# Performance work log

Measured on AMD Instinct MI355X. Metric: run time of the kernel, lower is better.

Reference implementation:

```python
import math
import jax, jax.numpy as jnp
import numpy as np

B, S, D, H = 2, 2048, 1024, 16


def setup_inputs() -> dict:
    key = jax.random.key(0)
    ks = jax.random.split(key, 8)
    scale = 1.0 / math.sqrt(D)
    kv_mask = jax.random.randint(ks[1], (B, S), 0, 2).astype(bool)
    kv_mask = kv_mask.at[:, 0].set(True)  # ensure at least one valid kv per batch
    return {
        "q": jax.random.normal(ks[0], (B, S, D), dtype=jnp.float32),
        "kv_mask": kv_mask,
        "Wq": jax.random.normal(ks[2], (D, D), dtype=jnp.float32) * scale,
        "Wk": jax.random.normal(ks[3], (D, D), dtype=jnp.float32) * scale,
        "Wv": jax.random.normal(ks[4], (D, D), dtype=jnp.float32) * scale,
        "Wo": jax.random.normal(ks[5], (D, D), dtype=jnp.float32) * scale,
        "bo": jax.random.normal(ks[6], (D,), dtype=jnp.float32) * 0.01,
        "num_heads": H,
    }


def _pass_with_mask(x, W, mask, b=None):
    # Linear applied everywhere, output zeroed where mask is False (pass_with_mask)
    y = x @ W.T
    if b is not None:
        y = y + b
    return jnp.where(mask[..., None], y, 0.0)


def reference(q, kv_mask, Wq, Wk, Wv, Wo, bo, num_heads):
    b, s, d = q.shape
    hd = d // num_heads
    q_mask = jnp.ones((b, s), dtype=bool)  # default q_mask in the module
    # self-attention: k = v = q
    qh = _pass_with_mask(q, Wq, q_mask).reshape(b, s, num_heads, hd)
    kh = _pass_with_mask(q, Wk, kv_mask).reshape(b, s, num_heads, hd)
    vh = _pass_with_mask(q, Wv, kv_mask).reshape(b, s, num_heads, hd)
    # scores: note the module scales by sqrt(model_dim), NOT sqrt(head_dim)
    scores = jnp.einsum("bqhd,bkhd->bhqk", qh, kh) / math.sqrt(d)
    mask = (q_mask[:, :, None] & kv_mask[:, None, :])[:, None, :, :]  # [b,1,q,k]
    scores = jnp.where(mask, scores, -jnp.inf)
    attn = jax.nn.softmax(scores, axis=-1)
    attn = jnp.where(mask, attn, 0.0)
    out = jnp.einsum("bhqk,bkhd->bqhd", attn, vh).reshape(b, s, d)
    return _pass_with_mask(out, Wo, q_mask, bo)
```

## Files before the change

### kernel.cpp

```cpp
#include <hip/hip_runtime.h>
#include <math.h>

#define B_ 2
#define S_ 2048
#define DM 1024
#define NH 16
#define HD 64

typedef unsigned short u16;
typedef unsigned int u32;
typedef __attribute__((ext_vector_type(8))) short bf16x8;
typedef __attribute__((ext_vector_type(4))) float f32x4;

#define C2SCALE 0.0450842200277800f

__device__ __forceinline__ u16 f2bf(float x) {
  unsigned u = __float_as_uint(x);
  u = (u + 0x7FFFu + ((u >> 16) & 1u)) >> 16;
  return (u16)u;
}

__device__ __forceinline__ u32 cvtpk(float lo, float hi) {
  u32 r;
  asm("v_cvt_pk_bf16_f32 %0, %1, %2" : "=v"(r) : "v"(lo), "v"(hi));
  return r;
}

__device__ __forceinline__ float exp2a(float x) {
  float r;
  asm("v_exp_f32 %0, %1" : "=v"(r) : "v"(x));
  return r;
}

__device__ __forceinline__ void gload_lds16(const u16* g, u16* l) {
  __builtin_amdgcn_global_load_lds((const __attribute__((address_space(1))) void*)g,
                                   (__attribute__((address_space(3))) void*)l, 16, 0, 0);
}

__device__ __forceinline__ int sigpos(int w6) {
  return ((w6 >> 5) << 5) | (((w6 >> 2) & 3) << 3) | (((w6 >> 4) & 1) << 2) | (w6 & 3);
}

__global__ void mask_scan(const int* __restrict__ kvm, int* __restrict__ posb,
                          int* __restrict__ nvb, u16* __restrict__ mwg) {
  const int b = blockIdx.x;
  const int tid = threadIdx.x;
  const int lane = tid & 63, wv = tid >> 6;
  __shared__ int wsum[4];
  int v[8], s = 0;
  const int base = b * S_ + tid * 8;
#pragma unroll
  for (int j = 0; j < 8; j++) { v[j] = kvm[base + j] ? 1 : 0; s += v[j]; }
  int sc = s;
#pragma unroll
  for (int off = 1; off < 64; off <<= 1) {
    int t = __shfl_up(sc, off, 64);
    if (lane >= off) sc += t;
  }
  if (lane == 63) wsum[wv] = sc;
  __syncthreads();
  int woff = 0;
#pragma unroll
  for (int w = 0; w < 4; w++) woff += (w < wv) ? wsum[w] : 0;
  int run = woff + sc - s;
#pragma unroll
  for (int j = 0; j < 8; j++) { posb[base + j] = run; run += v[j]; }
  const int total = wsum[0] + wsum[1] + wsum[2] + wsum[3];
  if (tid == 0) nvb[b] = total;
  for (int i = tid; i < S_; i += 256)
    mwg[b * S_ + (i & ~63) + sigpos(i & 63)] = (i < total) ? 0xFFFFu : 0u;
}

__global__ void cvt_all(const float* __restrict__ q, const float* __restrict__ Wq,
                        const float* __restrict__ Wk, const float* __restrict__ Wv,
                        const float* __restrict__ Wo, const int* __restrict__ kvm,
                        const int* __restrict__ posb, const int* __restrict__ nvb,
                        u16* __restrict__ Xbf, u16* __restrict__ Wcat,
                        u16* __restrict__ Wobf, u16* __restrict__ vtbuf,
                        u16* __restrict__ Xc) {
  const int NQ4 = (B_ * S_ * DM) / 4;
  const int NW4 = (DM * DM) / 4;
  const int total = NQ4 + 4 * NW4;
  int i = blockIdx.x * blockDim.x + threadIdx.x;
  int stride = gridDim.x * blockDim.x;
  for (int idx = i; idx < B_ * NH * HD * 64; idx += stride) {
    int col = idx & 63;
    int dd = (idx >> 6) & 63;
    int bh = idx >> 12;
    int nv = nvb[bh >> 4];
    int padw = ((nv + 63) & ~63) - nv;
    if (col < padw)
      vtbuf[((size_t)bh * HD + dd) * S_ + nv + col] = 0;
  }
  for (; i < total; i += stride) {
    if (i < NQ4) {
      float4 v = ((const float4*)q)[i];
      ushort4 o;
      o.x = f2bf(v.x); o.y = f2bf(v.y); o.z = f2bf(v.z); o.w = f2bf(v.w);
      ((ushort4*)Xbf)[i] = o;
      int row = i >> 8, chunk = i & 255;
      int b = row >> 11, s = row & 2047;
      if (kvm[b * S_ + s]) {
        int p = posb[b * S_ + s];
        *(ushort4*)(Xc + ((size_t)(b * S_ + p)) * DM + chunk * 4) = o;
      }
    } else {
      int t = i - NQ4;
      const float* src;
      u16* dst;
      if (t < NW4)            { src = Wq + (size_t)t * 4; dst = Wcat + (size_t)t * 4; }
      else if (t < 2 * NW4)   { src = Wk + (size_t)(t - NW4) * 4;     dst = Wcat + DM * DM + (size_t)(t - NW4) * 4; }
      else if (t < 3 * NW4)   { src = Wv + (size_t)(t - 2 * NW4) * 4; dst = Wcat + 2 * DM * DM + (size_t)(t - 2 * NW4) * 4; }
      else                    { src = Wo + (size_t)(t - 3 * NW4) * 4; dst = Wobf + (size_t)(t - 3 * NW4) * 4; }
      float4 v = *(const float4*)src;
      ushort4 o;
      o.x = f2bf(v.x); o.y = f2bf(v.y); o.z = f2bf(v.z); o.w = f2bf(v.w);
      *(ushort4*)dst = o;
    }
  }
}

__global__ __launch_bounds__(512, 4) void gemm_qkv(
    const u16* __restrict__ Xbf, const u16* __restrict__ Xc,
    const u16* __restrict__ Wcat, u16* __restrict__ qo, u16* __restrict__ ko,
    u16* __restrict__ vo, const int* __restrict__ nvb) {
  const int K = DM;
  const int Lraw = blockIdx.x;
  const int Ls = (Lraw & 7) * 96 + (Lraw >> 3);

  int Mb, nglob, bkv = 0, nv = 1 << 30;
  const u16* Ap;
  if (Ls < 256) {
    Mb = (Ls & 31) << 7;
    nglob = (Ls >> 5) << 7;
    Ap = Xbf;
  } else {
    int L2 = Ls - 256;
    bkv = L2 >> 8;
    int L3 = L2 & 255;
    Mb = (L3 & 15) << 7;
    nglob = 1024 + ((L3 >> 4) << 7);
    nv = nvb[bkv];
    if (Mb >= nv) return;
    Ap = Xc + (size_t)bkv * S_ * DM;
  }

  __shared__ __align__(16) u16 As[2][128 * 64];
  __shared__ __align__(16) u16 Bs[2][128 * 64];
  const int tid = threadIdx.x;
  const int wv = tid >> 6, lane = tid & 63;
  const int g = lane >> 4, c = lane & 15;
  const int wr = wv >> 1, wc = wv & 1;

  f32x4 acc[2][4];
#pragma unroll
  for (int i = 0; i < 2; i++)
#pragma unroll
    for (int j = 0; j < 4; j++) acc[i][j] = f32x4{0.f, 0.f, 0.f, 0.f};

  const int r1 = tid >> 3;
  const int col8 = tid & 7;
  const u16* ag1 = Ap + (size_t)(Mb + r1) * K + col8 * 8;
  const u16* ag2 = ag1 + (size_t)64 * K;
  const u16* bg1 = Wcat + (size_t)(nglob + r1) * K + col8 * 8;
  const u16* bg2 = bg1 + (size_t)64 * K;
  const int slot = col8 ^ (r1 & 7);
  u16* al1 = &As[0][r1 * 64 + slot * 8];
  u16* al2 = al1 + 64 * 64;
  u16* bl1 = &Bs[0][r1 * 64 + slot * 8];
  u16* bl2 = bl1 + 64 * 64;

  bf16x8 ar0 = *(const bf16x8*)ag1, ar1 = *(const bf16x8*)ag2;
  bf16x8 br0 = *(const bf16x8*)bg1, br1 = *(const bf16x8*)bg2;
  *(bf16x8*)al1 = ar0; *(bf16x8*)al2 = ar1;
  *(bf16x8*)bl1 = br0; *(bf16x8*)bl2 = br1;
  ar0 = *(const bf16x8*)(ag1 + 64); ar1 = *(const bf16x8*)(ag2 + 64);
  br0 = *(const bf16x8*)(bg1 + 64); br1 = *(const bf16x8*)(bg2 + 64);
  __syncthreads();

  const int swz = c & 7;
  const int NTI = 16;

  for (int t = 0; t < NTI; ++t) {
    const int cur = t & 1;
    if (t + 1 < NTI) {
      const int nb = (cur ^ 1) * 8192;
      *(bf16x8*)(al1 + nb) = ar0; *(bf16x8*)(al2 + nb) = ar1;
      *(bf16x8*)(bl1 + nb) = br0; *(bf16x8*)(bl2 + nb) = br1;
      if (t + 2 < NTI) {
        ar0 = *(const bf16x8*)(ag1 + (t + 2) * 64);
        ar1 = *(const bf16x8*)(ag2 + (t + 2) * 64);
        br0 = *(const bf16x8*)(bg1 + (t + 2) * 64);
        br1 = *(const bf16x8*)(bg2 + (t + 2) * 64);
      }
    }
    const u16* AB = &As[cur][0];
    const u16* BB = &Bs[cur][0];
#pragma unroll
    for (int ks = 0; ks < 2; ks++) {
      const int koff = ((4 * ks + g) ^ swz) * 8;
      bf16x8 af[2], bfr[4];
#pragma unroll
      for (int mi = 0; mi < 2; mi++)
        af[mi] = *(const bf16x8*)&AB[(wr * 32 + mi * 16 + c) * 64 + koff];
#pragma unroll
      for (int ni = 0; ni < 4; ni++)
        bfr[ni] = *(const bf16x8*)&BB[(wc * 64 + ni * 16 + c) * 64 + koff];
#pragma unroll
      for (int mi = 0; mi < 2; mi++)
#pragma unroll
        for (int ni = 0; ni < 4; ni++)
          acc[mi][ni] = __builtin_amdgcn_mfma_f32_16x16x32_bf16(af[mi], bfr[ni], acc[mi][ni], 0, 0, 0);
    }
    asm volatile("s_waitcnt lgkmcnt(0)\n\ts_barrier" ::: "memory");
  }

  const int nbase = nglob + wc * 64 + c;
  const int which = nbase >> 10;
  if (which == 0) {
#pragma unroll
    for (int mi = 0; mi < 2; mi++) {
#pragma unroll
      for (int ni = 0; ni < 4; ni++) {
        int nn = nbase + ni * 16;
        int h = nn >> 6, d = nn & 63;
#pragma unroll
        for (int r = 0; r < 4; r++) {
          int row = Mb + wr * 32 + mi * 16 + g * 4 + r;
          int b0 = row >> 11, s0 = row & 2047;
          qo[(((size_t)(b0 * NH + h)) * S_ + s0) * HD + d] =
              f2bf(acc[mi][ni][r] * C2SCALE);
        }
      }
    }
  } else if (which == 1) {
#pragma unroll
    for (int mi = 0; mi < 2; mi++) {
#pragma unroll
      for (int r = 0; r < 4; r++) {
        int p = Mb + wr * 32 + mi * 16 + g * 4 + r;
        if (p < nv) {
#pragma unroll
          for (int ni = 0; ni < 4; ni++) {
            int nn = (nbase + ni * 16) & 1023;
            ko[((size_t)(bkv * NH + (nn >> 6)) * S_ + p) * HD + (nn & 63)] =
                f2bf(acc[mi][ni][r]);
          }
        }
      }
    }
  } else {
#pragma unroll
    for (int mi = 0; mi < 2; mi++) {
#pragma unroll
      for (int r = 0; r < 4; r++) {
        int p = Mb + wr * 32 + mi * 16 + g * 4 + r;
        if (p < nv) {
          int dst = (p & ~63) + sigpos(p & 63);
#pragma unroll
          for (int ni = 0; ni < 4; ni++) {
            int nn = (nbase + ni * 16) & 1023;
            vo[((size_t)((bkv * NH + (nn >> 6)) * HD + (nn & 63))) * S_ + dst] =
                f2bf(acc[mi][ni][r]);
          }
        }
      }
    }
  }
}

__global__ __launch_bounds__(256, 4) void gemm_n64(
    const u16* __restrict__ A, const u16* __restrict__ Bw,
    const float* __restrict__ bias, float* __restrict__ fo) {
  __shared__ __align__(16) u16 As[128 * 32];
  __shared__ __align__(16) u16 Bs[64 * 32];
  const int K = DM, N = DM;
  const int tid = threadIdx.x;
  const int wv = tid >> 6, lane = tid & 63;
  const int g = lane >> 4, c = lane & 15;
  const int wr = wv >> 1, wc = wv & 1;
  const int L = blockIdx.x;
  const int Ls = (L & 7) * 64 + (L >> 3);
  const int Mb = (Ls & 31) << 7, Nb = (Ls >> 5) << 6;

  f32x4 acc[4][2];
#pragma unroll
  for (int i = 0; i < 4; i++)
#pragma unroll
    for (int j = 0; j < 2; j++) acc[i][j] = f32x4{0.f, 0.f, 0.f, 0.f};

  for (int kb = 0; kb < K; kb += 32) {
#pragma unroll
    for (int it = 0; it < 2; ++it) {
      int id = it * 256 + tid;
      int m = id >> 2, kk = (id & 3) * 8;
      gload_lds16(A + (size_t)(Mb + m) * K + kb + kk, As + (it * 4 + wv) * 512);
    }
    {
      int m = tid >> 2, kk = (tid & 3) * 8;
      gload_lds16(Bw + (size_t)(Nb + m) * K + kb + kk, Bs + wv * 512);
    }
    __syncthreads();
    bf16x8 af[4], bfr[2];
#pragma unroll
    for (int mi = 0; mi < 4; mi++)
      af[mi] = *(const bf16x8*)(As + (wr * 64 + mi * 16 + c) * 32 + g * 8);
#pragma unroll
    for (int ni = 0; ni < 2; ni++)
      bfr[ni] = *(const bf16x8*)(Bs + (wc * 32 + ni * 16 + c) * 32 + g * 8);
#pragma unroll
    for (int mi = 0; mi < 4; mi++)
#pragma unroll
      for (int ni = 0; ni < 2; ni++)
        acc[mi][ni] = __builtin_amdgcn_mfma_f32_16x16x32_bf16(af[mi], bfr[ni], acc[mi][ni], 0, 0, 0);
    __syncthreads();
  }

#pragma unroll
  for (int mi = 0; mi < 4; mi++) {
#pragma unroll
    for (int ni = 0; ni < 2; ni++) {
      int n = Nb + wc * 32 + ni * 16 + c;
      float bv = bias[n];
#pragma unroll
      for (int r = 0; r < 4; r++) {
        int row = Mb + wr * 64 + mi * 16 + g * 4 + r;
        fo[(size_t)row * N + n] = acc[mi][ni][r] + bv;
      }
    }
  }
}

__global__ __launch_bounds__(256, 3) void attn_kernel(
    const u16* __restrict__ qb, const u16* __restrict__ kb,
    const u16* __restrict__ vtb, const u16* __restrict__ mwg,
    const int* __restrict__ nvb, u16* __restrict__ ob) {
  __shared__ __align__(16) u16 Kl[2][64 * 64];
  __shared__ __align__(16) u16 Vl[2][64 * 64];
  __shared__ __align__(16) u16 MW[S_];

  const int tid = threadIdx.x;
  const int wv = tid >> 6, lane = tid & 63;
  const int g = lane >> 4, c = lane & 15;

  const int L = blockIdx.x;
  const int j = L >> 3;
  const int bh = ((L & 7) << 2) | (j >> 4);
  const int qi = j & 15;
  const int b = bh >> 4, h = bh & 15;
  const int q0 = qi * 128;
  const size_t bhbase = (size_t)bh * (S_ * HD);
  const int NT = (nvb[b] + 63) >> 6;

  ((uint4*)MW)[tid] = ((const uint4*)(mwg + b * S_))[tid];

  bf16x8 qf[2][2];
#pragma unroll
  for (int mi = 0; mi < 2; mi++)
#pragma unroll
    for (int ks = 0; ks < 2; ks++)
      qf[mi][ks] = *(const bf16x8*)(qb + bhbase +
                   (size_t)(q0 + wv * 32 + mi * 16 + c) * HD + ks * 32 + g * 8);

  f32x4 Oa[4][2];
#pragma unroll
  for (int di = 0; di < 4; di++)
#pragma unroll
    for (int mi = 0; mi < 2; mi++) Oa[di][mi] = f32x4{0.f, 0.f, 0.f, 0.f};
  f32x4 lacc[2];
  lacc[0] = f32x4{0.f, 0.f, 0.f, 0.f};
  lacc[1] = f32x4{0.f, 0.f, 0.f, 0.f};

  union { u32 u[4]; bf16x8 v; } ones;
#pragma unroll
  for (int w = 0; w < 4; w++) ones.u[w] = 0x3F803F80u;

  const int srow = tid >> 3;
  const int scol8 = tid & 7;
  const u16* kg1 = kb + bhbase + (size_t)srow * HD + scol8 * 8;
  const u16* kg2 = kg1 + (size_t)32 * HD;
  const u16* vg1 = vtb + bhbase + (size_t)srow * S_ + scol8 * 8;
  const u16* vg2 = vg1 + (size_t)32 * S_;
  const int wslot = scol8 ^ (srow & 7);
  u16* kld1 = &Kl[0][srow * 64 + wslot * 8];
  u16* kld2 = kld1 + 32 * 64;
  u16* vld1 = &Vl[0][srow * 64 + wslot * 8];
  u16* vld2 = vld1 + 32 * 64;

  bf16x8 krg[2], vrg[2];
  krg[0] = *(const bf16x8*)kg1;  krg[1] = *(const bf16x8*)kg2;
  vrg[0] = *(const bf16x8*)vg1;  vrg[1] = *(const bf16x8*)vg2;
  *(bf16x8*)kld1 = krg[0];  *(bf16x8*)kld2 = krg[1];
  *(bf16x8*)vld1 = vrg[0];  *(bf16x8*)vld2 = vrg[1];
  krg[0] = *(const bf16x8*)(kg1 + 4096);  krg[1] = *(const bf16x8*)(kg2 + 4096);
  vrg[0] = *(const bf16x8*)(vg1 + 64);    vrg[1] = *(const bf16x8*)(vg2 + 64);
  __syncthreads();

  const int swz = c & 7;

  for (int t = 0; t < NT; ++t) {
    const int cur = t & 1;
    if (t + 1 < NT) {
      const int nb = (cur ^ 1) * 4096;
      *(bf16x8*)(kld1 + nb) = krg[0];  *(bf16x8*)(kld2 + nb) = krg[1];
      *(bf16x8*)(vld1 + nb) = vrg[0];  *(bf16x8*)(vld2 + nb) = vrg[1];
      if (t + 2 < NT) {
        krg[0] = *(const bf16x8*)(kg1 + (t + 2) * 4096);
        krg[1] = *(const bf16x8*)(kg2 + (t + 2) * 4096);
        vrg[0] = *(const bf16x8*)(vg1 + (t + 2) * 64);
        vrg[1] = *(const bf16x8*)(vg2 + (t + 2) * 64);
      }
    }
    const u16* KB = &Kl[cur][0];
    const u16* VB = &Vl[cur][0];

    f32x4 Sa[4][2];
#pragma unroll
    for (int ni = 0; ni < 4; ni++)
#pragma unroll
      for (int mi = 0; mi < 2; mi++) Sa[ni][mi] = f32x4{0.f, 0.f, 0.f, 0.f};
    __builtin_amdgcn_s_setprio(1);
#pragma unroll
    for (int ks = 0; ks < 2; ks++) {
      bf16x8 kf[4];
#pragma unroll
      for (int ni = 0; ni < 4; ni++)
        kf[ni] = *(const bf16x8*)&KB[(ni * 16 + c) * 64 + (((4 * ks + g) ^ swz) * 8)];
#pragma unroll
      for (int ni = 0; ni < 4; ni++)
#pragma unroll
        for (int mi = 0; mi < 2; mi++)
          Sa[ni][mi] = __builtin_amdgcn_mfma_f32_16x16x32_bf16(kf[ni], qf[mi][ks], Sa[ni][mi], 0, 0, 0);
    }
    __builtin_amdgcn_s_setprio(0);

    bf16x8 Pa[2][2];
#pragma unroll
    for (int ks = 0; ks < 2; ks++) {
      uint4 mw = *(const uint4*)&MW[t * 64 + ks * 32 + g * 8];
#pragma unroll
      for (int mi = 0; mi < 2; mi++) {
        union { u32 u[4]; bf16x8 v; } pw;
        pw.u[0] = cvtpk(exp2a(Sa[2 * ks][mi][0]), exp2a(Sa[2 * ks][mi][1])) & mw.x;
        pw.u[1] = cvtpk(exp2a(Sa[2 * ks][mi][2]), exp2a(Sa[2 * ks][mi][3])) & mw.y;
        pw.u[2] = cvtpk(exp2a(Sa[2 * ks + 1][mi][0]), exp2a(Sa[2 * ks + 1][mi][1])) & mw.z;
        pw.u[3] = cvtpk(exp2a(Sa[2 * ks + 1][mi][2]), exp2a(Sa[2 * ks + 1][mi][3])) & mw.w;
        Pa[mi][ks] = pw.v;
      }
    }

    __builtin_amdgcn_s_setprio(1);
#pragma unroll
    for (int mi = 0; mi < 2; mi++) {
      lacc[mi] = __builtin_amdgcn_mfma_f32_16x16x32_bf16(ones.v, Pa[mi][0], lacc[mi], 0, 0, 0);
      lacc[mi] = __builtin_amdgcn_mfma_f32_16x16x32_bf16(ones.v, Pa[mi][1], lacc[mi], 0, 0, 0);
    }
#pragma unroll
    for (int ks = 0; ks < 2; ks++) {
      bf16x8 vf[4];
#pragma unroll
      for (int di = 0; di < 4; di++)
        vf[di] = *(const bf16x8*)&VB[(di * 16 + c) * 64 + (((4 * ks + g) ^ swz) * 8)];
#pragma unroll
      for (int di = 0; di < 4; di++)
#pragma unroll
        for (int mi = 0; mi < 2; mi++)
          Oa[di][mi] = __builtin_amdgcn_mfma_f32_16x16x32_bf16(vf[di], Pa[mi][ks], Oa[di][mi], 0, 0, 0);
    }
    __builtin_amdgcn_s_setprio(0);

    asm volatile("s_waitcnt lgkmcnt(0)\n\ts_barrier" ::: "memory");
  }

#pragma unroll
  for (int mi = 0; mi < 2; mi++) {
    float inv = 1.f / lacc[mi][0];
    int q = q0 + wv * 32 + mi * 16 + c;
    size_t base = ((size_t)(b * S_ + q)) * DM + (size_t)h * HD;
#pragma unroll
    for (int di = 0; di < 4; di++) {
      uint2 o;
      o.x = cvtpk(Oa[di][mi][0] * inv, Oa[di][mi][1] * inv);
      o.y = cvtpk(Oa[di][mi][2] * inv, Oa[di][mi][3] * inv);
      *(uint2*)(ob + base + di * 16 + g * 4) = o;
    }
  }
}

extern "C" void kernel_launch(void* const* d_in, const int* in_sizes, int n_in,
                              void* d_out, int out_size, void* d_ws, size_t ws_size,
                              hipStream_t stream) {
  const float* q  = (const float*)d_in[0];
  const int* kvm  = (const int*)d_in[1];
  const float* Wq = (const float*)d_in[2];
  const float* Wk = (const float*)d_in[3];
  const float* Wv = (const float*)d_in[4];
  const float* Wo = (const float*)d_in[5];
  const float* bo = (const float*)d_in[6];
  float* out = (float*)d_out;
  char* ws = (char*)d_ws;

  u16* Xbf   = (u16*)(ws);
  u16* Wcat  = (u16*)(ws + (8u << 20));
  u16* Wobf  = (u16*)(ws + (14u << 20));
  u16* qbuf  = (u16*)(ws + (16u << 20));
  u16* kbuf  = (u16*)(ws + (24u << 20));
  u16* vtbuf = (u16*)(ws + (32u << 20));
  u16* mwg   = (u16*)(ws + (40u << 20));
  int* posb  = (int*)(ws + (41u << 20));
  int* nvb   = (int*)(ws + (42u << 20));
  u16* Xc    = (u16*)d_out;
  u16* obuf  = Xbf;

  mask_scan<<<B_, 256, 0, stream>>>(kvm, posb, nvb, mwg);
  cvt_all<<<2048, 256, 0, stream>>>(q, Wq, Wk, Wv, Wo, kvm, posb, nvb,
                                    Xbf, Wcat, Wobf, vtbuf, Xc);
  gemm_qkv<<<768, 512, 0, stream>>>(Xbf, Xc, Wcat, qbuf, kbuf, vtbuf, nvb);
  attn_kernel<<<512, 256, 0, stream>>>(qbuf, kbuf, vtbuf, mwg, nvb, obuf);
  gemm_n64<<<512, 256, 0, stream>>>(obuf, Wobf, bo, out);
}
```

Before: 101.2 us.

## Split attention KV range across two blocks and merge partial outputs

Each (batch, head, query-tile) is now processed by two blocks, each covering half of the valid KV tiles, doubling the attention grid. Unnormalized partial outputs and row sums are written to scratch, and a new merge kernel sums them, normalizes, and writes the combined head output. This aims to improve CU occupancy and load balance, at the cost of an extra kernel launch, extra memory traffic, and bf16 rounding of the partial outputs. The launch bound also rises to 4 blocks per CU.

```diff
diff --git a/kernel.cpp b/kernel.cpp
--- a/kernel.cpp
+++ b/kernel.cpp
@@ -30,6 +30,10 @@
   float r;
   asm("v_exp_f32 %0, %1" : "=v"(r) : "v"(x));
   return r;
+}
+
+__device__ __forceinline__ float bf2f(u16 v) {
+  return __uint_as_float(((u32)v) << 16);
 }
 
 __device__ __forceinline__ void gload_lds16(const u16* g, u16* l) {
@@ -331,10 +335,10 @@
   }
 }
 
-__global__ __launch_bounds__(256, 3) void attn_kernel(
+__global__ __launch_bounds__(256, 4) void attn_kernel(
     const u16* __restrict__ qb, const u16* __restrict__ kb,
     const u16* __restrict__ vtb, const u16* __restrict__ mwg,
-    const int* __restrict__ nvb, u16* __restrict__ ob) {
+    const int* __restrict__ nvb, u16* __restrict__ op, float* __restrict__ lbuf) {
   __shared__ __align__(16) u16 Kl[2][64 * 64];
   __shared__ __align__(16) u16 Vl[2][64 * 64];
   __shared__ __align__(16) u16 MW[S_];
@@ -345,12 +349,15 @@
 
   const int L = blockIdx.x;
   const int j = L >> 3;
-  const int bh = ((L & 7) << 2) | (j >> 4);
-  const int qi = j & 15;
-  const int b = bh >> 4, h = bh & 15;
+  const int bh = ((L & 7) << 2) | (j >> 5);
+  const int qi = (j >> 1) & 15;
+  const int half = j & 1;
+  const int b = bh >> 4;
   const int q0 = qi * 128;
   const size_t bhbase = (size_t)bh * (S_ * HD);
   const int NT = (nvb[b] + 63) >> 6;
+  const int t0 = half ? ((NT + 1) >> 1) : 0;
+  const int tend = half ? NT : ((NT + 1) >> 1);
 
   ((uint4*)MW)[tid] = ((const uint4*)(mwg + b * S_))[tid];
 
@@ -377,9 +384,9 @@
 
   const int srow = tid >> 3;
   const int scol8 = tid & 7;
-  const u16* kg1 = kb + bhbase + (size_t)srow * HD + scol8 * 8;
+  const u16* kg1 = kb + bhbase + (size_t)srow * HD + scol8 * 8 + (size_t)t0 * 4096;
   const u16* kg2 = kg1 + (size_t)32 * HD;
-  const u16* vg1 = vtb + bhbase + (size_t)srow * S_ + scol8 * 8;
+  const u16* vg1 = vtb + bhbase + (size_t)srow * S_ + scol8 * 8 + (size_t)t0 * 64;
   const u16* vg2 = vg1 + (size_t)32 * S_;
   const int wslot = scol8 ^ (srow & 7);
   u16* kld1 = &Kl[0][srow * 64 + wslot * 8];
@@ -398,17 +405,17 @@
 
   const int swz = c & 7;
 
-  for (int t = 0; t < NT; ++t) {
-    const int cur = t & 1;
-    if (t + 1 < NT) {
+  for (int t = t0; t < tend; ++t) {
+    const int cur = (t - t0) & 1;
+    if (t + 1 < tend) {
       const int nb = (cur ^ 1) * 4096;
       *(bf16x8*)(kld1 + nb) = krg[0];  *(bf16x8*)(kld2 + nb) = krg[1];
       *(bf16x8*)(vld1 + nb) = vrg[0];  *(bf16x8*)(vld2 + nb) = vrg[1];
-      if (t + 2 < NT) {
-        krg[0] = *(const bf16x8*)(kg1 + (t + 2) * 4096);
-        krg[1] = *(const bf16x8*)(kg2 + (t + 2) * 4096);
-        vrg[0] = *(const bf16x8*)(vg1 + (t + 2) * 64);
-        vrg[1] = *(const bf16x8*)(vg2 + (t + 2) * 64);
+      if (t + 2 < tend) {
+        krg[0] = *(const bf16x8*)(kg1 + (t + 2 - t0) * 4096);
+        krg[1] = *(const bf16x8*)(kg2 + (t + 2 - t0) * 4096);
+        vrg[0] = *(const bf16x8*)(vg1 + (t + 2 - t0) * 64);
+        vrg[1] = *(const bf16x8*)(vg2 + (t + 2 - t0) * 64);
       }
     }
     const u16* KB = &Kl[cur][0];
@@ -474,17 +481,42 @@
 
 #pragma unroll
   for (int mi = 0; mi < 2; mi++) {
-    float inv = 1.f / lacc[mi][0];
     int q = q0 + wv * 32 + mi * 16 + c;
-    size_t base = ((size_t)(b * S_ + q)) * DM + (size_t)h * HD;
+    size_t base = ((size_t)((half * 32 + bh) * S_ + q)) * 64;
 #pragma unroll
     for (int di = 0; di < 4; di++) {
       uint2 o;
-      o.x = cvtpk(Oa[di][mi][0] * inv, Oa[di][mi][1] * inv);
-      o.y = cvtpk(Oa[di][mi][2] * inv, Oa[di][mi][3] * inv);
-      *(uint2*)(ob + base + di * 16 + g * 4) = o;
-    }
-  }
+      o.x = cvtpk(Oa[di][mi][0], Oa[di][mi][1]);
+      o.y = cvtpk(Oa[di][mi][2], Oa[di][mi][3]);
+      *(uint2*)(op + base + di * 16 + g * 4) = o;
+    }
+    if (g == 0)
+      lbuf[(size_t)(half * 32 + bh) * S_ + q] = lacc[mi][0];
+  }
+}
+
+__global__ void merge_o(const u16* __restrict__ op, const float* __restrict__ lbuf,
+                        u16* __restrict__ acomb) {
+  int id = blockIdx.x * blockDim.x + threadIdx.x;
+  int d8 = id & 7;
+  int q = (id >> 3) & (S_ - 1);
+  int bh = id >> 14;
+  int b = bh >> 4, h = bh & 15;
+  size_t r1 = ((size_t)(bh * S_ + q)) * 64 + d8 * 8;
+  size_t r2 = r1 + (size_t)32 * S_ * 64;
+  float l1 = lbuf[(size_t)bh * S_ + q];
+  float l2 = lbuf[(size_t)(32 + bh) * S_ + q];
+  float rl = 1.f / (l1 + l2);
+  bf16x8 o1 = *(const bf16x8*)(op + r1);
+  bf16x8 o2 = *(const bf16x8*)(op + r2);
+  union { u32 u[4]; bf16x8 v; } res;
+#pragma unroll
+  for (int jj = 0; jj < 4; jj++) {
+    float lo = (bf2f((u16)o1[2 * jj]) + bf2f((u16)o2[2 * jj])) * rl;
+    float hi = (bf2f((u16)o1[2 * jj + 1]) + bf2f((u16)o2[2 * jj + 1])) * rl;
+    res.u[jj] = cvtpk(lo, hi);
+  }
+  *(bf16x8*)(acomb + ((size_t)(b * S_ + q)) * DM + h * HD + d8 * 8) = res.v;
 }
 
 extern "C" void kernel_launch(void* const* d_in, const int* in_sizes, int n_in,
@@ -509,13 +541,16 @@
   u16* mwg   = (u16*)(ws + (40u << 20));
   int* posb  = (int*)(ws + (41u << 20));
   int* nvb   = (int*)(ws + (42u << 20));
+  float* lbuf = (float*)(ws + (43u << 20));
   u16* Xc    = (u16*)d_out;
+  u16* opart = (u16*)d_out;
   u16* obuf  = Xbf;
 
   mask_scan<<<B_, 256, 0, stream>>>(kvm, posb, nvb, mwg);
   cvt_all<<<2048, 256, 0, stream>>>(q, Wq, Wk, Wv, Wo, kvm, posb, nvb,
                                     Xbf, Wcat, Wobf, vtbuf, Xc);
   gemm_qkv<<<768, 512, 0, stream>>>(Xbf, Xc, Wcat, qbuf, kbuf, vtbuf, nvb);
-  attn_kernel<<<512, 256, 0, stream>>>(qbuf, kbuf, vtbuf, mwg, nvb, obuf);
+  attn_kernel<<<1024, 256, 0, stream>>>(qbuf, kbuf, vtbuf, mwg, nvb, opart, lbuf);
+  merge_o<<<2048, 256, 0, stream>>>(opart, lbuf, obuf);
   gemm_n64<<<512, 256, 0, stream>>>(obuf, Wobf, bo, out);
 }
```

Measured after the change: 106.7 us. 5.3% more time.

## Double-buffer output-projection GEMM with register prefetch and XOR-swizzled LDS

Applied to the files above, without the earlier changes.

Rewrites the gemm_n64 main loop to use K-tiles of 64 with two LDS buffers. Global loads go to registers two tiles ahead and are stored into the alternate buffer, which leaves one barrier per iteration instead of two. An XOR swizzle on the LDS layout is meant to avoid bank conflicts on the fragment reads. LDS use grows to 48KB, so occupancy is lowered to 3 blocks per CU. The hand-written barrier relies on waitcnt semantics for correctness.

```diff
diff --git a/kernel.cpp b/kernel.cpp
--- a/kernel.cpp
+++ b/kernel.cpp
@@ -269,11 +269,11 @@
   }
 }
 
-__global__ __launch_bounds__(256, 4) void gemm_n64(
+__global__ __launch_bounds__(256, 3) void gemm_n64(
     const u16* __restrict__ A, const u16* __restrict__ Bw,
     const float* __restrict__ bias, float* __restrict__ fo) {
-  __shared__ __align__(16) u16 As[128 * 32];
-  __shared__ __align__(16) u16 Bs[64 * 32];
+  __shared__ __align__(16) u16 As[2][128 * 64];
+  __shared__ __align__(16) u16 Bs[2][64 * 64];
   const int K = DM, N = DM;
   const int tid = threadIdx.x;
   const int wv = tid >> 6, lane = tid & 63;
@@ -289,31 +289,72 @@
 #pragma unroll
     for (int j = 0; j < 2; j++) acc[i][j] = f32x4{0.f, 0.f, 0.f, 0.f};
 
-  for (int kb = 0; kb < K; kb += 32) {
-#pragma unroll
-    for (int it = 0; it < 2; ++it) {
-      int id = it * 256 + tid;
-      int m = id >> 2, kk = (id & 3) * 8;
-      gload_lds16(A + (size_t)(Mb + m) * K + kb + kk, As + (it * 4 + wv) * 512);
-    }
-    {
-      int m = tid >> 2, kk = (tid & 3) * 8;
-      gload_lds16(Bw + (size_t)(Nb + m) * K + kb + kk, Bs + wv * 512);
-    }
-    __syncthreads();
-    bf16x8 af[4], bfr[2];
-#pragma unroll
-    for (int mi = 0; mi < 4; mi++)
-      af[mi] = *(const bf16x8*)(As + (wr * 64 + mi * 16 + c) * 32 + g * 8);
-#pragma unroll
-    for (int ni = 0; ni < 2; ni++)
-      bfr[ni] = *(const bf16x8*)(Bs + (wc * 32 + ni * 16 + c) * 32 + g * 8);
-#pragma unroll
-    for (int mi = 0; mi < 4; mi++)
+  const int r0 = tid >> 3;
+  const int col8 = tid & 7;
+  const int slot = col8 ^ (r0 & 7);
+  const u16* ag0 = A + (size_t)(Mb + r0) * K + col8 * 8;
+  const u16* ag1 = ag0 + (size_t)32 * K;
+  const u16* ag2 = ag0 + (size_t)64 * K;
+  const u16* ag3 = ag0 + (size_t)96 * K;
+  const u16* bg0 = Bw + (size_t)(Nb + r0) * K + col8 * 8;
+  const u16* bg1 = bg0 + (size_t)32 * K;
+  u16* al0 = &As[0][r0 * 64 + slot * 8];
+  u16* al1 = al0 + 32 * 64;
+  u16* al2 = al0 + 64 * 64;
+  u16* al3 = al0 + 96 * 64;
+  u16* bl0 = &Bs[0][r0 * 64 + slot * 8];
+  u16* bl1 = bl0 + 32 * 64;
+
+  bf16x8 arA = *(const bf16x8*)ag0, arB = *(const bf16x8*)ag1;
+  bf16x8 arC = *(const bf16x8*)ag2, arD = *(const bf16x8*)ag3;
+  bf16x8 brA = *(const bf16x8*)bg0, brB = *(const bf16x8*)bg1;
+  *(bf16x8*)al0 = arA; *(bf16x8*)al1 = arB;
+  *(bf16x8*)al2 = arC; *(bf16x8*)al3 = arD;
+  *(bf16x8*)bl0 = brA; *(bf16x8*)bl1 = brB;
+  arA = *(const bf16x8*)(ag0 + 64); arB = *(const bf16x8*)(ag1 + 64);
+  arC = *(const bf16x8*)(ag2 + 64); arD = *(const bf16x8*)(ag3 + 64);
+  brA = *(const bf16x8*)(bg0 + 64); brB = *(const bf16x8*)(bg1 + 64);
+  __syncthreads();
+
+  const int swz = c & 7;
+  const int NTI = 16;
+
+  for (int t = 0; t < NTI; ++t) {
+    const int cur = t & 1;
+    if (t + 1 < NTI) {
+      const int nbA = (cur ^ 1) * 8192;
+      const int nbB = (cur ^ 1) * 4096;
+      *(bf16x8*)(al0 + nbA) = arA; *(bf16x8*)(al1 + nbA) = arB;
+      *(bf16x8*)(al2 + nbA) = arC; *(bf16x8*)(al3 + nbA) = arD;
+      *(bf16x8*)(bl0 + nbB) = brA; *(bf16x8*)(bl1 + nbB) = brB;
+      if (t + 2 < NTI) {
+        arA = *(const bf16x8*)(ag0 + (t + 2) * 64);
+        arB = *(const bf16x8*)(ag1 + (t + 2) * 64);
+        arC = *(const bf16x8*)(ag2 + (t + 2) * 64);
+        arD = *(const bf16x8*)(ag3 + (t + 2) * 64);
+        brA = *(const bf16x8*)(bg0 + (t + 2) * 64);
+        brB = *(const bf16x8*)(bg1 + (t + 2) * 64);
+      }
+    }
+    const u16* AB = &As[cur][0];
+    const u16* BB = &Bs[cur][0];
+#pragma unroll
+    for (int ks = 0; ks < 2; ks++) {
+      const int koff = ((4 * ks + g) ^ swz) * 8;
+      bf16x8 af[4], bfr[2];
+#pragma unroll
+      for (int mi = 0; mi < 4; mi++)
+        af[mi] = *(const bf16x8*)&AB[(wr * 64 + mi * 16 + c) * 64 + koff];
 #pragma unroll
       for (int ni = 0; ni < 2; ni++)
-        acc[mi][ni] = __builtin_amdgcn_mfma_f32_16x16x32_bf16(af[mi], bfr[ni], acc[mi][ni], 0, 0, 0);
-    __syncthreads();
+        bfr[ni] = *(const bf16x8*)&BB[(wc * 32 + ni * 16 + c) * 64 + koff];
+#pragma unroll
+      for (int mi = 0; mi < 4; mi++)
+#pragma unroll
+        for (int ni = 0; ni < 2; ni++)
+          acc[mi][ni] = __builtin_amdgcn_mfma_f32_16x16x32_bf16(af[mi], bfr[ni], acc[mi][ni], 0, 0, 0);
+    }
+    asm volatile("s_waitcnt lgkmcnt(0)\n\ts_barrier" ::: "memory");
   }
 
 #pragma unroll
```

New measurement: 97.83 us (median of 2 runs). 1.03x faster.

## Use direct global-to-LDS loads in QKV GEMM, output GEMM and attention

Applied to the files above, without the earlier changes.

Replaces the register-staged prefetch (global load into VGPRs, then LDS store) in the QKV projection GEMM and the attention K/V tile loop with direct global-to-LDS 16-byte loads. The swizzle moves to the global source address so the LDS layout stays the same. The output GEMM is also restructured into a double-buffered 64-wide K-step pipeline with swizzled LDS and direct loads, lowering its occupancy hint from 4 to 3 to fit the larger shared memory. The goal is to cut VGPR pressure and LDS store instructions and to overlap loads with MFMA work; the cost is relying on full __syncthreads waits for vmcnt, which may serialize loads.

```diff
diff --git a/kernel.cpp b/kernel.cpp
--- a/kernel.cpp
+++ b/kernel.cpp
@@ -158,24 +158,23 @@
 #pragma unroll
     for (int j = 0; j < 4; j++) acc[i][j] = f32x4{0.f, 0.f, 0.f, 0.f};
 
-  const int r1 = tid >> 3;
-  const int col8 = tid & 7;
-  const u16* ag1 = Ap + (size_t)(Mb + r1) * K + col8 * 8;
-  const u16* ag2 = ag1 + (size_t)64 * K;
-  const u16* bg1 = Wcat + (size_t)(nglob + r1) * K + col8 * 8;
-  const u16* bg2 = bg1 + (size_t)64 * K;
-  const int slot = col8 ^ (r1 & 7);
-  u16* al1 = &As[0][r1 * 64 + slot * 8];
-  u16* al2 = al1 + 64 * 64;
-  u16* bl1 = &Bs[0][r1 * 64 + slot * 8];
-  u16* bl2 = bl1 + 64 * 64;
-
-  bf16x8 ar0 = *(const bf16x8*)ag1, ar1 = *(const bf16x8*)ag2;
-  bf16x8 br0 = *(const bf16x8*)bg1, br1 = *(const bf16x8*)bg2;
-  *(bf16x8*)al1 = ar0; *(bf16x8*)al2 = ar1;
-  *(bf16x8*)bl1 = br0; *(bf16x8*)bl2 = br1;
-  ar0 = *(const bf16x8*)(ag1 + 64); ar1 = *(const bf16x8*)(ag2 + 64);
-  br0 = *(const bf16x8*)(bg1 + 64); br1 = *(const bf16x8*)(bg2 + 64);
+  const int lrow = lane >> 3;
+  const int lchk = (lane & 7) ^ (lrow & 7);
+  const int r0a = (0 * 8 + wv) * 8 + lrow;
+  const int r1a = (1 * 8 + wv) * 8 + lrow;
+  const u16* agS0 = Ap + (size_t)(Mb + r0a) * K + lchk * 8;
+  const u16* agS1 = Ap + (size_t)(Mb + r1a) * K + lchk * 8;
+  const u16* bgS0 = Wcat + (size_t)(nglob + r0a) * K + lchk * 8;
+  const u16* bgS1 = Wcat + (size_t)(nglob + r1a) * K + lchk * 8;
+  u16* alB0 = &As[0][(0 * 8 + wv) * 512];
+  u16* alB1 = &As[0][(1 * 8 + wv) * 512];
+  u16* blB0 = &Bs[0][(0 * 8 + wv) * 512];
+  u16* blB1 = &Bs[0][(1 * 8 + wv) * 512];
+
+  gload_lds16(agS0, alB0);
+  gload_lds16(agS1, alB1);
+  gload_lds16(bgS0, blB0);
+  gload_lds16(bgS1, blB1);
   __syncthreads();
 
   const int swz = c & 7;
@@ -185,14 +184,11 @@
     const int cur = t & 1;
     if (t + 1 < NTI) {
       const int nb = (cur ^ 1) * 8192;
-      *(bf16x8*)(al1 + nb) = ar0; *(bf16x8*)(al2 + nb) = ar1;
-      *(bf16x8*)(bl1 + nb) = br0; *(bf16x8*)(bl2 + nb) = br1;
-      if (t + 2 < NTI) {
-        ar0 = *(const bf16x8*)(ag1 + (t + 2) * 64);
-        ar1 = *(const bf16x8*)(ag2 + (t + 2) * 64);
-        br0 = *(const bf16x8*)(bg1 + (t + 2) * 64);
-        br1 = *(const bf16x8*)(bg2 + (t + 2) * 64);
-      }
+      const int go = (t + 1) * 64;
+      gload_lds16(agS0 + go, alB0 + nb);
+      gload_lds16(agS1 + go, alB1 + nb);
+      gload_lds16(bgS0 + go, blB0 + nb);
+      gload_lds16(bgS1 + go, blB1 + nb);
     }
     const u16* AB = &As[cur][0];
     const u16* BB = &Bs[cur][0];
@@ -212,7 +208,7 @@
         for (int ni = 0; ni < 4; ni++)
           acc[mi][ni] = __builtin_amdgcn_mfma_f32_16x16x32_bf16(af[mi], bfr[ni], acc[mi][ni], 0, 0, 0);
     }
-    asm volatile("s_waitcnt lgkmcnt(0)\n\ts_barrier" ::: "memory");
+    __syncthreads();
   }
 
   const int nbase = nglob + wc * 64 + c;
@@ -269,11 +265,11 @@
   }
 }
 
-__global__ __launch_bounds__(256, 4) void gemm_n64(
+__global__ __launch_bounds__(256, 3) void gemm_n64(
     const u16* __restrict__ A, const u16* __restrict__ Bw,
     const float* __restrict__ bias, float* __restrict__ fo) {
-  __shared__ __align__(16) u16 As[128 * 32];
-  __shared__ __align__(16) u16 Bs[64 * 32];
+  __shared__ __align__(16) u16 As[2][128 * 64];
+  __shared__ __align__(16) u16 Bs[2][64 * 64];
   const int K = DM, N = DM;
   const int tid = threadIdx.x;
   const int wv = tid >> 6, lane = tid & 63;
@@ -289,30 +285,61 @@
 #pragma unroll
     for (int j = 0; j < 2; j++) acc[i][j] = f32x4{0.f, 0.f, 0.f, 0.f};
 
-  for (int kb = 0; kb < K; kb += 32) {
-#pragma unroll
-    for (int it = 0; it < 2; ++it) {
-      int id = it * 256 + tid;
-      int m = id >> 2, kk = (id & 3) * 8;
-      gload_lds16(A + (size_t)(Mb + m) * K + kb + kk, As + (it * 4 + wv) * 512);
-    }
-    {
-      int m = tid >> 2, kk = (tid & 3) * 8;
-      gload_lds16(Bw + (size_t)(Nb + m) * K + kb + kk, Bs + wv * 512);
-    }
-    __syncthreads();
-    bf16x8 af[4], bfr[2];
-#pragma unroll
-    for (int mi = 0; mi < 4; mi++)
-      af[mi] = *(const bf16x8*)(As + (wr * 64 + mi * 16 + c) * 32 + g * 8);
-#pragma unroll
-    for (int ni = 0; ni < 2; ni++)
-      bfr[ni] = *(const bf16x8*)(Bs + (wc * 32 + ni * 16 + c) * 32 + g * 8);
-#pragma unroll
-    for (int mi = 0; mi < 4; mi++)
+  const int lrow = lane >> 3;
+  const int lchk = (lane & 7) ^ (lrow & 7);
+  const u16* agS[4];
+  u16* alB[4];
+#pragma unroll
+  for (int cl = 0; cl < 4; cl++) {
+    agS[cl] = A + (size_t)(Mb + (cl * 4 + wv) * 8 + lrow) * K + lchk * 8;
+    alB[cl] = &As[0][(cl * 4 + wv) * 512];
+  }
+  const u16* bgS[2];
+  u16* blB[2];
+#pragma unroll
+  for (int cl = 0; cl < 2; cl++) {
+    bgS[cl] = Bw + (size_t)(Nb + (cl * 4 + wv) * 8 + lrow) * K + lchk * 8;
+    blB[cl] = &Bs[0][(cl * 4 + wv) * 512];
+  }
+
+#pragma unroll
+  for (int cl = 0; cl < 4; cl++) gload_lds16(agS[cl], alB[cl]);
+#pragma unroll
+  for (int cl = 0; cl < 2; cl++) gload_lds16(bgS[cl], blB[cl]);
+  __syncthreads();
+
+  const int swz = c & 7;
+  const int NTI = 16;
+
+  for (int t = 0; t < NTI; ++t) {
+    const int cur = t & 1;
+    if (t + 1 < NTI) {
+      const int nbA = (cur ^ 1) * 8192;
+      const int nbB = (cur ^ 1) * 4096;
+      const int go = (t + 1) * 64;
+#pragma unroll
+      for (int cl = 0; cl < 4; cl++) gload_lds16(agS[cl] + go, alB[cl] + nbA);
+#pragma unroll
+      for (int cl = 0; cl < 2; cl++) gload_lds16(bgS[cl] + go, blB[cl] + nbB);
+    }
+    const u16* AB = &As[cur][0];
+    const u16* BB = &Bs[cur][0];
+#pragma unroll
+    for (int ks = 0; ks < 2; ks++) {
+      const int koff = ((4 * ks + g) ^ swz) * 8;
+      bf16x8 af[4], bfr[2];
+#pragma unroll
+      for (int mi = 0; mi < 4; mi++)
+        af[mi] = *(const bf16x8*)&AB[(wr * 64 + mi * 16 + c) * 64 + koff];
 #pragma unroll
       for (int ni = 0; ni < 2; ni++)
-        acc[mi][ni] = __builtin_amdgcn_mfma_f32_16x16x32_bf16(af[mi], bfr[ni], acc[mi][ni], 0, 0, 0);
+        bfr[ni] = *(const bf16x8*)&BB[(wc * 32 + ni * 16 + c) * 64 + koff];
+#pragma unroll
+      for (int mi = 0; mi < 4; mi++)
+#pragma unroll
+        for (int ni = 0; ni < 2; ni++)
+          acc[mi][ni] = __builtin_amdgcn_mfma_f32_16x16x32_bf16(af[mi], bfr[ni], acc[mi][ni], 0, 0, 0);
+    }
     __syncthreads();
   }
 
@@ -375,25 +402,23 @@
 #pragma unroll
   for (int w = 0; w < 4; w++) ones.u[w] = 0x3F803F80u;
 
-  const int srow = tid >> 3;
-  const int scol8 = tid & 7;
-  const u16* kg1 = kb + bhbase + (size_t)srow * HD + scol8 * 8;
-  const u16* kg2 = kg1 + (size_t)32 * HD;
-  const u16* vg1 = vtb + bhbase + (size_t)srow * S_ + scol8 * 8;
-  const u16* vg2 = vg1 + (size_t)32 * S_;
-  const int wslot = scol8 ^ (srow & 7);
-  u16* kld1 = &Kl[0][srow * 64 + wslot * 8];
-  u16* kld2 = kld1 + 32 * 64;
-  u16* vld1 = &Vl[0][srow * 64 + wslot * 8];
-  u16* vld2 = vld1 + 32 * 64;
-
-  bf16x8 krg[2], vrg[2];
-  krg[0] = *(const bf16x8*)kg1;  krg[1] = *(const bf16x8*)kg2;
-  vrg[0] = *(const bf16x8*)vg1;  vrg[1] = *(const bf16x8*)vg2;
-  *(bf16x8*)kld1 = krg[0];  *(bf16x8*)kld2 = krg[1];
-  *(bf16x8*)vld1 = vrg[0];  *(bf16x8*)vld2 = vrg[1];
-  krg[0] = *(const bf16x8*)(kg1 + 4096);  krg[1] = *(const bf16x8*)(kg2 + 4096);
-  vrg[0] = *(const bf16x8*)(vg1 + 64);    vrg[1] = *(const bf16x8*)(vg2 + 64);
+  const int lrow = lane >> 3;
+  const int lchk = (lane & 7) ^ (lrow & 7);
+  const int kr0 = (0 * 4 + wv) * 8 + lrow;
+  const int kr1 = (1 * 4 + wv) * 8 + lrow;
+  const u16* kgS0 = kb + bhbase + (size_t)kr0 * HD + lchk * 8;
+  const u16* kgS1 = kb + bhbase + (size_t)kr1 * HD + lchk * 8;
+  const u16* vgS0 = vtb + bhbase + (size_t)kr0 * S_ + lchk * 8;
+  const u16* vgS1 = vtb + bhbase + (size_t)kr1 * S_ + lchk * 8;
+  u16* klB0 = &Kl[0][(0 * 4 + wv) * 512];
+  u16* klB1 = &Kl[0][(1 * 4 + wv) * 512];
+  u16* vlB0 = &Vl[0][(0 * 4 + wv) * 512];
+  u16* vlB1 = &Vl[0][(1 * 4 + wv) * 512];
+
+  gload_lds16(kgS0, klB0);
+  gload_lds16(kgS1, klB1);
+  gload_lds16(vgS0, vlB0);
+  gload_lds16(vgS1, vlB1);
   __syncthreads();
 
   const int swz = c & 7;
@@ -402,14 +427,10 @@
     const int cur = t & 1;
     if (t + 1 < NT) {
       const int nb = (cur ^ 1) * 4096;
-      *(bf16x8*)(kld1 + nb) = krg[0];  *(bf16x8*)(kld2 + nb) = krg[1];
-      *(bf16x8*)(vld1 + nb) = vrg[0];  *(bf16x8*)(vld2 + nb) = vrg[1];
-      if (t + 2 < NT) {
-        krg[0] = *(const bf16x8*)(kg1 + (t + 2) * 4096);
-        krg[1] = *(const bf16x8*)(kg2 + (t + 2) * 4096);
-        vrg[0] = *(const bf16x8*)(vg1 + (t + 2) * 64);
-        vrg[1] = *(const bf16x8*)(vg2 + (t + 2) * 64);
-      }
+      gload_lds16(kgS0 + (t + 1) * 4096, klB0 + nb);
+      gload_lds16(kgS1 + (t + 1) * 4096, klB1 + nb);
+      gload_lds16(vgS0 + (t + 1) * 64, vlB0 + nb);
+      gload_lds16(vgS1 + (t + 1) * 64, vlB1 + nb);
     }
     const u16* KB = &Kl[cur][0];
     const u16* VB = &Vl[cur][0];
@@ -469,7 +490,7 @@
     }
     __builtin_amdgcn_s_setprio(0);
 
-    asm volatile("s_waitcnt lgkmcnt(0)\n\ts_barrier" ::: "memory");
+    __syncthreads();
   }
 
 #pragma unroll
```

Measured after the change: 106.4 us. 5.1% more time.
